# Kernel optimization log

Hardware: AMD Instinct MI355X
Metric: run time of the kernel (lower is better)

The kernel has to match this reference:

```python
import jax, jax.numpy as jnp
import numpy as np

N_NODES = 10000
N_EDGES = 30000
NODE_DIM = 75
BOND_DIM = 16
IN_DIM = 64           # nn_conv_in_dim (also NNConv out channels)
INTERNAL = 128        # nn_conv_internal_dim
FP_DIM = 4096
N_GRAPHS = 16
DEPTH = 3


def _glorot(key, shape):
    fan_in = shape[0]
    return jax.random.normal(key, shape, dtype=jnp.float32) / np.sqrt(fan_in)


def setup_inputs() -> dict:
    key = jax.random.key(0)
    ks = jax.random.split(key, 16)
    x = jax.random.normal(ks[0], (N_NODES, NODE_DIM), dtype=jnp.float32)
    edge_index = jax.random.randint(ks[1], (2, N_EDGES), 0, N_NODES, dtype=jnp.int32)
    edge_attr = jax.random.uniform(ks[2], (N_EDGES, BOND_DIM), dtype=jnp.float32)
    # last column is the bond type flag: 0 = covalent, 1 = spatial
    bond_type = jax.random.randint(ks[3], (N_EDGES,), 0, 2).astype(jnp.float32)
    edge_attr = edge_attr.at[:, -1].set(bond_type)
    batch = jnp.sort(jax.random.randint(ks[4], (N_NODES,), 0, N_GRAPHS, dtype=jnp.int32))
    return {
        "x": x,
        "edge_index": edge_index,
        "edge_attr": edge_attr,
        "batch": batch,
        # atom_expand_nn: Linear(node_dim, nn_conv_in_dim) + ReLU
        "W_ae": _glorot(ks[5], (NODE_DIM, IN_DIM)),
        "b_ae": jnp.zeros((IN_DIM,), jnp.float32),
        # NNConv edge MLP: Linear(bond_dim, internal) -> ReLU -> Linear(internal, in*in)
        "W_e1": _glorot(ks[6], (BOND_DIM, INTERNAL)),
        "b_e1": jnp.zeros((INTERNAL,), jnp.float32),
        "W_e2": _glorot(ks[7], (INTERNAL, IN_DIM * IN_DIM)),
        "b_e2": jnp.zeros((IN_DIM * IN_DIM,), jnp.float32),
        # NNConv root weight + bias
        "W_root": _glorot(ks[8], (IN_DIM, IN_DIM)),
        "b_conv": jnp.zeros((IN_DIM,), jnp.float32),
        # expand_to_fp_nn: Linear(nn_conv_in_dim, fp_dim) + ReLU
        "W_fp": _glorot(ks[9], (IN_DIM, FP_DIM)),
        "b_fp": jnp.zeros((FP_DIM,), jnp.float32),
    }


def reference(x, edge_index, edge_attr, batch,
              W_ae, b_ae, W_e1, b_e1, W_e2, b_e2, W_root, b_conv, W_fp, b_fp):
    src, dst = edge_index[0], edge_index[1]
    cov_mask = (edge_attr[:, -1] == 0.0).astype(x.dtype)   # [E]
    spa_mask = 1.0 - cov_mask

    msg = jax.nn.relu(x @ W_ae + b_ae)                      # [N, IN]
    fingerprint = jnp.zeros((FP_DIM,), x.dtype)

    def masked_mean_aggr(per_edge_msg, mask):
        # NNConv aggregation on the masked edge subset (mean over incoming edges)
        s = jax.ops.segment_sum(per_edge_msg * mask[:, None], dst, num_segments=N_NODES)
        cnt = jax.ops.segment_sum(mask, dst, num_segments=N_NODES)
        return jnp.where(cnt[:, None] > 0, s / jnp.maximum(cnt, 1.0)[:, None], 0.0)

    for _ in range(DEPTH):
        # edge MLP -> per-edge [IN, IN] weight matrix (dropout inactive at eval)
        h = jax.nn.relu(edge_attr @ W_e1 + b_e1)            # [E, INTERNAL]
        w = (h @ W_e2 + b_e2).reshape(N_EDGES, IN_DIM, IN_DIM)
        # gather source features and apply per-edge matrix
        per_edge = jnp.einsum('ei,eio->eo', msg[src], w)    # [E, IN]
        root = msg @ W_root + b_conv                        # [N, IN]
        cov_out = masked_mean_aggr(per_edge, cov_mask) + root
        spa_out = masked_mean_aggr(per_edge, spa_mask) + root
        msg = jax.nn.relu(cov_out + spa_out)
        # expand_to_fp_nn includes ReLU; outer F.relu is idempotent
        expanded = jax.nn.relu(msg @ W_fp + b_fp)           # [N, FP]
        pooled = jax.ops.segment_sum(expanded, batch, num_segments=N_GRAPHS)  # add pool
        # sparsify = identity; skip_connections=True accumulates every depth
        fingerprint = fingerprint + pooled
    return fingerprint                                      # [N_GRAPHS, FP_DIM]
```

## Files before the change

kernel.cpp:

```cpp
#include <hip/hip_runtime.h>
#include <hip/hip_fp16.h>

#define N_NODES 10000
#define N_EDGES 30000
#define NODE_DIM 75
#define BOND_DIM 16
#define IN_DIM 64
#define INTERNAL 128
#define FP_DIM 4096
#define N_GRAPHS 16
#define DEPTH 3

typedef _Float16 half8v __attribute__((ext_vector_type(8)));
typedef float float4v __attribute__((ext_vector_type(4)));

__global__ void k_atom_expand(const float* __restrict__ x, const float* __restrict__ W,
                              const float* __restrict__ b, float* __restrict__ msg,
                              __half* __restrict__ msg16) {
    int n = blockIdx.x;
    int o = threadIdx.x;
    __shared__ float xr[NODE_DIM];
    if (o < NODE_DIM) xr[o] = x[(size_t)n * NODE_DIM + o];
    if (o + 64 < NODE_DIM) xr[o + 64] = x[(size_t)n * NODE_DIM + o + 64];
    __syncthreads();
    float acc = b[o];
    #pragma unroll
    for (int k = 0; k < NODE_DIM; ++k) acc = fmaf(xr[k], W[k * IN_DIM + o], acc);
    float v = fmaxf(acc, 0.f);
    msg[(size_t)n * IN_DIM + o] = v;
    msg16[(size_t)n * IN_DIM + o] = __float2half(v);
}

__global__ void k_edge_h16(const float* __restrict__ ea, const float* __restrict__ W1,
                           const float* __restrict__ b1, __half* __restrict__ h,
                           const int* __restrict__ dst,
                           float* __restrict__ cntC, float* __restrict__ cntS,
                           const int* __restrict__ batch, int* __restrict__ gstart,
                           float* __restrict__ agg0) {
    const int tid = threadIdx.x;
    const int q = tid >> 7;
    const int j = tid & 127;
    const int e = blockIdx.x * 2 + q;
    __shared__ float r[2][BOND_DIM];
    if (j < BOND_DIM) r[q][j] = ea[(size_t)e * BOND_DIM + j];

    if (blockIdx.x < 1250)
        ((float2*)agg0)[(size_t)blockIdx.x * 256 + tid] = (float2){0.f, 0.f};
    if (blockIdx.x == 0 && tid <= N_GRAPHS) {
        int g = tid, lo = 0, hi = N_NODES;
        while (lo < hi) { int mid = (lo + hi) >> 1; if (batch[mid] < g) lo = mid + 1; else hi = mid; }
        gstart[g] = lo;
    }
    __syncthreads();
    if (j == 0) {
        if (r[q][BOND_DIM - 1] == 0.f) atomicAdd(&cntC[dst[e]], 1.f);
        else                           atomicAdd(&cntS[dst[e]], 1.f);
    }
    float acc = b1[j];
    #pragma unroll
    for (int k = 0; k < BOND_DIM; ++k) acc = fmaf(r[q][k], W1[k * INTERNAL + j], acc);
    h[(size_t)e * INTERNAL + j] = __float2half(fmaxf(acc, 0.f));
}

__global__ void k_w2t(const float* __restrict__ W2, __half* __restrict__ W2T) {
    __shared__ _Float16 t[64][136];
    const int tid = threadIdx.x;
    const int n0 = blockIdx.x * 64;
    #pragma unroll
    for (int i = 0; i < 32; ++i) {
        int k = (tid >> 6) + 4 * i;
        int n = tid & 63;
        t[n][k] = (_Float16)W2[(size_t)k * 4096 + n0 + n];
    }
    __syncthreads();
    const int nr = tid >> 2;
    const int kc = (tid & 3) * 32;
    _Float16* dstp = (_Float16*)W2T + (size_t)(n0 + nr) * INTERNAL + kc;
    const _Float16* srcp = &t[nr][kc];
    #pragma unroll
    for (int j = 0; j < 4; ++j)
        *(half8v*)(dstp + 8 * j) = *(const half8v*)(srcp + 8 * j);
}

__global__ void k_wfpt(const float* __restrict__ Wfp, __half* __restrict__ WfpT) {
    __shared__ _Float16 t[64][80];
    const int tid = threadIdx.x;
    const int n0 = blockIdx.x * 64;
    #pragma unroll
    for (int i = 0; i < 16; ++i) {
        int k = (tid >> 6) + 4 * i;
        int n = tid & 63;
        t[n][k] = (_Float16)Wfp[(size_t)k * 4096 + n0 + n];
    }
    __syncthreads();
    const int nr = tid >> 2;
    const int kc = (tid & 3) * 16;
    _Float16* dstp = (_Float16*)WfpT + (size_t)(n0 + nr) * IN_DIM + kc;
    const _Float16* srcp = &t[nr][kc];
    *(half8v*)(dstp)     = *(const half8v*)(srcp);
    *(half8v*)(dstp + 8) = *(const half8v*)(srcp + 8);
}

__global__ __launch_bounds__(512) void k_wgemm(
    const __half* __restrict__ h16, const __half* __restrict__ W2T,
    const float* __restrict__ b2, __half* __restrict__ w)
{
    __shared__ _Float16 B[128][136];
    __shared__ _Float16 st[8][16][136];
    const int tid  = threadIdx.x;
    const int lane = tid & 63;
    const int wv   = tid >> 6;
    const int nbase = blockIdx.x * 128;
    const int ebase = blockIdx.y * 256 + wv * 32;
    const int l15 = lane & 15;
    const int kq  = (lane >> 4) * 8;

    const _Float16* hp = (const _Float16*)h16;
    const _Float16* wp = (const _Float16*)W2T;

    half8v a[2][4];
    #pragma unroll
    for (int mi = 0; mi < 2; ++mi) {
        int e = ebase + mi * 16 + l15;
        if (e >= N_EDGES) e = N_EDGES - 1;
        const _Float16* arow = hp + (size_t)e * INTERNAL;
        #pragma unroll
        for (int kk = 0; kk < 4; ++kk)
            a[mi][kk] = *(const half8v*)(arow + kk * 32 + kq);
    }
    float bias[8];
    #pragma unroll
    for (int ni = 0; ni < 8; ++ni) bias[ni] = b2[nbase + ni * 16 + l15];

    {
        int r  = tid >> 2;
        int c0 = (tid & 3) * 32;
        const _Float16* srcp = wp + (size_t)(nbase + r) * INTERNAL + c0;
        *(half8v*)&B[r][c0]      = *(const half8v*)(srcp);
        *(half8v*)&B[r][c0 + 8]  = *(const half8v*)(srcp + 8);
        *(half8v*)&B[r][c0 + 16] = *(const half8v*)(srcp + 16);
        *(half8v*)&B[r][c0 + 24] = *(const half8v*)(srcp + 24);
    }
    __syncthreads();

    float4v acc[2][8];
    #pragma unroll
    for (int mi = 0; mi < 2; ++mi)
        #pragma unroll
        for (int ni = 0; ni < 8; ++ni)
            acc[mi][ni] = (float4v){0.f, 0.f, 0.f, 0.f};

    #pragma unroll
    for (int kk = 0; kk < 4; ++kk) {
        half8v bw[8];
        #pragma unroll
        for (int ni = 0; ni < 8; ++ni)
            bw[ni] = *(const half8v*)&B[ni * 16 + l15][kk * 32 + kq];
        #pragma unroll
        for (int ni = 0; ni < 8; ++ni) {
            acc[0][ni] = __builtin_amdgcn_mfma_f32_16x16x32_f16(a[0][kk], bw[ni], acc[0][ni], 0, 0, 0);
            acc[1][ni] = __builtin_amdgcn_mfma_f32_16x16x32_f16(a[1][kk], bw[ni], acc[1][ni], 0, 0, 0);
        }
    }

    const int rq = (lane >> 4) * 4;
    #pragma unroll
    for (int mi = 0; mi < 2; ++mi) {
        #pragma unroll
        for (int ni = 0; ni < 8; ++ni)
            #pragma unroll
            for (int r = 0; r < 4; ++r)
                st[wv][rq + r][ni * 16 + l15] = (_Float16)(acc[mi][ni][r] + bias[ni]);
        #pragma unroll
        for (int it = 0; it < 4; ++it) {
            int erow = it * 4 + (lane >> 4);
            half8v v = *(const half8v*)&st[wv][erow][l15 * 8];
            int e = ebase + mi * 16 + erow;
            if (e < N_EDGES)
                *(half8v*)((_Float16*)w + (size_t)e * FP_DIM + nbase + l15 * 8) = v;
        }
    }
}

__global__ __launch_bounds__(256) void k_edge_apply(
    const float* __restrict__ msg, const __half* __restrict__ w,
    const int* __restrict__ src, const int* __restrict__ dst,
    const float* __restrict__ ea,
    const float* __restrict__ cntC, const float* __restrict__ cntS,
    float* __restrict__ agg)
{
    const int lane = threadIdx.x & 63;
    const int ig = lane >> 3;
    const int oc = lane & 7;
    const int nw = (int)gridDim.x * 4;
    int e = (int)blockIdx.x * 4 + ((int)threadIdx.x >> 6);
    if (e >= N_EDGES) return;

    float mv = msg[(size_t)src[e] * IN_DIM + lane];
    half8v w8[8];
    {
        const half8v* wr = (const half8v*)((const _Float16*)w + (size_t)e * FP_DIM);
        #pragma unroll
        for (int t = 0; t < 8; ++t) w8[t] = wr[(ig + 8 * t) * 8 + oc];
    }
    int dv = dst[e];
    float scale = 1.0f / ((ea[(size_t)e * BOND_DIM + (BOND_DIM - 1)] == 0.f)
                          ? cntC[dv] : cntS[dv]);

    while (true) {
        const int en = e + nw;
        const bool has = (en < N_EDGES);
        float nmv = 0.f, nscale = 0.f;
        int ndv = 0;
        half8v n8[8];
        if (has) {
            nmv = msg[(size_t)src[en] * IN_DIM + lane];
            const half8v* wrn = (const half8v*)((const _Float16*)w + (size_t)en * FP_DIM);
            #pragma unroll
            for (int t = 0; t < 8; ++t) n8[t] = wrn[(ig + 8 * t) * 8 + oc];
            ndv = dst[en];
            nscale = 1.0f / ((ea[(size_t)en * BOND_DIM + (BOND_DIM - 1)] == 0.f)
                             ? cntC[ndv] : cntS[ndv]);
        }

        float acc[8] = {0.f, 0.f, 0.f, 0.f, 0.f, 0.f, 0.f, 0.f};
        #pragma unroll
        for (int t = 0; t < 8; ++t) {
            float mi = __shfl(mv, ig + 8 * t);
            #pragma unroll
            for (int j = 0; j < 8; ++j) acc[j] = fmaf(mi, (float)w8[t][j], acc[j]);
        }
        #pragma unroll
        for (int d = 8; d < 64; d <<= 1)
            #pragma unroll
            for (int j = 0; j < 8; ++j) acc[j] += __shfl_xor(acc[j], d);

        float v = (ig == 0) ? acc[0] : (ig == 1) ? acc[1] : (ig == 2) ? acc[2] :
                  (ig == 3) ? acc[3] : (ig == 4) ? acc[4] : (ig == 5) ? acc[5] :
                  (ig == 6) ? acc[6] : acc[7];
        atomicAdd(&agg[(size_t)dv * IN_DIM + oc * 8 + ig], v * scale);

        if (!has) break;
        e = en; mv = nmv; dv = ndv; scale = nscale;
        #pragma unroll
        for (int t = 0; t < 8; ++t) w8[t] = n8[t];
    }
}

__global__ void k_combine(const float* __restrict__ msg_old, const float* __restrict__ Wr,
                          const float* __restrict__ bc,
                          float* __restrict__ agg,
                          float* __restrict__ msg_new, __half* __restrict__ msg16) {
    int tid = threadIdx.x;
    int n = blockIdx.x * 4 + (tid >> 6);
    int o = tid & 63;
    int q = tid >> 6;
    __shared__ float r[4][IN_DIM];
    r[q][o] = msg_old[(size_t)n * IN_DIM + o];
    __syncthreads();
    float root = bc[o];
    #pragma unroll
    for (int k = 0; k < IN_DIM; ++k) root = fmaf(r[q][k], Wr[k * IN_DIM + o], root);
    size_t idx = (size_t)n * IN_DIM + o;
    float a = agg[idx];
    agg[idx] = 0.f;
    float v = fmaxf(a + 2.f * root, 0.f);
    msg_new[idx] = v;
    msg16[idx] = __float2half(v);
}

__global__ __launch_bounds__(256) void k_fp_pool_mfma(
    const __half* __restrict__ msg16, const __half* __restrict__ WfpT,
    const float* __restrict__ bfp, const int* __restrict__ gstart,
    float* __restrict__ out)
{
    const int tid = threadIdx.x, lane = tid & 63, wid = tid >> 6;
    const int g = blockIdx.y;
    const int cbase = blockIdx.x * 256 + wid * 64;
    const int l15 = lane & 15;
    const int kq = (lane >> 4) * 8;
    const int rq = (lane >> 4) * 4;

    const _Float16* wt = (const _Float16*)WfpT;
    const _Float16* mp = (const _Float16*)msg16;

    half8v bf[4][2];
    float bias[4];
    #pragma unroll
    for (int nf = 0; nf < 4; ++nf) {
        int n = cbase + nf * 16 + l15;
        #pragma unroll
        for (int kk = 0; kk < 2; ++kk)
            bf[nf][kk] = *(const half8v*)(wt + (size_t)n * IN_DIM + kk * 32 + kq);
        bias[nf] = bfp[n];
    }

    int n0g = gstart[g], n1g = gstart[g + 1];
    int len = n1g - n0g;
    int chunk = (len + (int)gridDim.z - 1) / (int)gridDim.z;
    int rs = n0g + (int)blockIdx.z * chunk;
    int re = min(rs + chunk, n1g);
    if (rs >= re) return;

    float pool[4] = {0.f, 0.f, 0.f, 0.f};
    int node0 = rs + l15; if (node0 >= n1g) node0 = n1g - 1;
    half8v af0 = *(const half8v*)(mp + (size_t)node0 * IN_DIM + kq);
    half8v af1 = *(const half8v*)(mp + (size_t)node0 * IN_DIM + 32 + kq);
    for (int r = rs; r < re; r += 16) {
        half8v nf0 = af0, nf1 = af1;
        if (r + 16 < re) {
            int node = r + 16 + l15; if (node >= n1g) node = n1g - 1;
            nf0 = *(const half8v*)(mp + (size_t)node * IN_DIM + kq);
            nf1 = *(const half8v*)(mp + (size_t)node * IN_DIM + 32 + kq);
        }
        #pragma unroll
        for (int nf = 0; nf < 4; ++nf) {
            float4v d = (float4v){0.f, 0.f, 0.f, 0.f};
            d = __builtin_amdgcn_mfma_f32_16x16x32_f16(af0, bf[nf][0], d, 0, 0, 0);
            d = __builtin_amdgcn_mfma_f32_16x16x32_f16(af1, bf[nf][1], d, 0, 0, 0);
            #pragma unroll
            for (int reg = 0; reg < 4; ++reg) {
                int rr = r + rq + reg;
                if (rr < re) pool[nf] += fmaxf(d[reg] + bias[nf], 0.f);
            }
        }
        af0 = nf0; af1 = nf1;
    }
    #pragma unroll
    for (int nf = 0; nf < 4; ++nf) {
        pool[nf] += __shfl_xor(pool[nf], 16);
        pool[nf] += __shfl_xor(pool[nf], 32);
    }
    if (lane < 16) {
        #pragma unroll
        for (int nf = 0; nf < 4; ++nf)
            atomicAdd(&out[(size_t)g * FP_DIM + cbase + nf * 16 + lane], pool[nf]);
    }
}

extern "C" void kernel_launch(void* const* d_in, const int* in_sizes, int n_in,
                              void* d_out, int out_size, void* d_ws, size_t ws_size,
                              hipStream_t stream) {
    const float* x        = (const float*)d_in[0];
    const int*   eidx     = (const int*)d_in[1];
    const float* ea       = (const float*)d_in[2];
    const int*   batch    = (const int*)d_in[3];
    const float* W_ae     = (const float*)d_in[4];
    const float* b_ae     = (const float*)d_in[5];
    const float* W_e1     = (const float*)d_in[6];
    const float* b_e1     = (const float*)d_in[7];
    const float* W_e2     = (const float*)d_in[8];
    const float* b_e2     = (const float*)d_in[9];
    const float* W_root   = (const float*)d_in[10];
    const float* b_conv   = (const float*)d_in[11];
    const float* W_fp     = (const float*)d_in[12];
    const float* b_fp     = (const float*)d_in[13];
    const int* src = eidx;
    const int* dst = eidx + N_EDGES;
    float* out = (float*)d_out;

    hipMemsetAsync(out, 0, (size_t)out_size * sizeof(float), stream);

    float* ws   = (float*)d_ws;
    float* msgA = ws;
    float* msgB = msgA + 640000;
    float* aggC = msgB + 640000;
    float* aggS = aggC + 640000;
    float* cntC = aggS + 640000;
    float* cntS = cntC + 10000;
    int*   gst  = (int*)(cntS + 10000);

    __half* h16   = (__half*)(gst + 32);
    __half* W2T   = h16 + (size_t)N_EDGES * INTERNAL;
    __half* wbig  = W2T + (size_t)FP_DIM * INTERNAL;
    __half* msg16 = wbig + (size_t)N_EDGES * FP_DIM;
    __half* WfpT  = msg16 + (size_t)N_NODES * IN_DIM;

    size_t need = (4ull * 640000 + 2 * 10000 + 32) * 4
                + ((size_t)N_EDGES * INTERNAL + (size_t)FP_DIM * INTERNAL
                   + (size_t)N_EDGES * FP_DIM + (size_t)N_NODES * IN_DIM
                   + (size_t)FP_DIM * IN_DIM) * 2;
    if (ws_size < need) return;

    hipMemsetAsync(cntC, 0, 2 * (size_t)N_NODES * sizeof(float), stream);
    k_atom_expand<<<N_NODES, 64, 0, stream>>>(x, W_ae, b_ae, msgA, msg16);
    k_edge_h16<<<N_EDGES / 2, 256, 0, stream>>>(ea, W_e1, b_e1, h16,
                                                dst, cntC, cntS, batch, gst, aggC);
    k_w2t<<<64, 256, 0, stream>>>(W_e2, W2T);
    k_wfpt<<<64, 256, 0, stream>>>(W_fp, WfpT);
    k_wgemm<<<dim3(FP_DIM / 128, (N_EDGES + 255) / 256), 512, 0, stream>>>(
        h16, W2T, b_e2, wbig);

    float* cur = msgA;
    float* nxt = msgB;
    for (int d = 0; d < DEPTH; ++d) {
        k_edge_apply<<<1024, 256, 0, stream>>>(
            cur, wbig, src, dst, ea, cntC, cntS, aggC);
        k_combine<<<N_NODES / 4, 256, 0, stream>>>(cur, W_root, b_conv, aggC,
                                                   nxt, msg16);
        k_fp_pool_mfma<<<dim3(FP_DIM / 256, N_GRAPHS, 8), 256, 0, stream>>>(
            msg16, WfpT, b_fp, gst, out);
        float* t = cur; cur = nxt; nxt = t;
    }
}
```

Baseline: 309.9 us.

## Batch node expand blocks, merge transposes, shrink staging, double-buffer edge apply

The atom-expand kernel now handles four nodes per 256-thread block instead of one node per 64-thread block. The two weight-transpose kernels are merged into one launch. The wgemm epilogue stages the output through a half-size shared buffer in four passes, which lowers LDS use and may allow more resident blocks. The edge-apply loop becomes a two-deep software pipeline with A/B register sets, and the fp-pool grid z dimension drops from 8 to 4. Together these aim to cut launch overhead, improve occupancy and hide load latency, at the cost of more registers in edge_apply.

```diff
diff --git a/kernel.cpp b/kernel.cpp
--- a/kernel.cpp
+++ b/kernel.cpp
@@ -17,15 +17,17 @@
 __global__ void k_atom_expand(const float* __restrict__ x, const float* __restrict__ W,
                               const float* __restrict__ b, float* __restrict__ msg,
                               __half* __restrict__ msg16) {
-    int n = blockIdx.x;
-    int o = threadIdx.x;
-    __shared__ float xr[NODE_DIM];
-    if (o < NODE_DIM) xr[o] = x[(size_t)n * NODE_DIM + o];
-    if (o + 64 < NODE_DIM) xr[o + 64] = x[(size_t)n * NODE_DIM + o + 64];
+    int tid = threadIdx.x;
+    int q = tid >> 6;
+    int o = tid & 63;
+    int n = blockIdx.x * 4 + q;
+    __shared__ float xr[4][NODE_DIM];
+    if (o < NODE_DIM) xr[q][o] = x[(size_t)n * NODE_DIM + o];
+    if (o + 64 < NODE_DIM) xr[q][o + 64] = x[(size_t)n * NODE_DIM + o + 64];
     __syncthreads();
     float acc = b[o];
     #pragma unroll
-    for (int k = 0; k < NODE_DIM; ++k) acc = fmaf(xr[k], W[k * IN_DIM + o], acc);
+    for (int k = 0; k < NODE_DIM; ++k) acc = fmaf(xr[q][k], W[k * IN_DIM + o], acc);
     float v = fmaxf(acc, 0.f);
     msg[(size_t)n * IN_DIM + o] = v;
     msg16[(size_t)n * IN_DIM + o] = __float2half(v);
@@ -62,43 +64,42 @@
     h[(size_t)e * INTERNAL + j] = __float2half(fmaxf(acc, 0.f));
 }
 
-__global__ void k_w2t(const float* __restrict__ W2, __half* __restrict__ W2T) {
+__global__ void k_wt(const float* __restrict__ W2, const float* __restrict__ Wfp,
+                     __half* __restrict__ W2T, __half* __restrict__ WfpT) {
     __shared__ _Float16 t[64][136];
     const int tid = threadIdx.x;
-    const int n0 = blockIdx.x * 64;
-    #pragma unroll
-    for (int i = 0; i < 32; ++i) {
-        int k = (tid >> 6) + 4 * i;
-        int n = tid & 63;
-        t[n][k] = (_Float16)W2[(size_t)k * 4096 + n0 + n];
-    }
-    __syncthreads();
-    const int nr = tid >> 2;
-    const int kc = (tid & 3) * 32;
-    _Float16* dstp = (_Float16*)W2T + (size_t)(n0 + nr) * INTERNAL + kc;
-    const _Float16* srcp = &t[nr][kc];
-    #pragma unroll
-    for (int j = 0; j < 4; ++j)
-        *(half8v*)(dstp + 8 * j) = *(const half8v*)(srcp + 8 * j);
-}
-
-__global__ void k_wfpt(const float* __restrict__ Wfp, __half* __restrict__ WfpT) {
-    __shared__ _Float16 t[64][80];
-    const int tid = threadIdx.x;
-    const int n0 = blockIdx.x * 64;
-    #pragma unroll
-    for (int i = 0; i < 16; ++i) {
-        int k = (tid >> 6) + 4 * i;
-        int n = tid & 63;
-        t[n][k] = (_Float16)Wfp[(size_t)k * 4096 + n0 + n];
-    }
-    __syncthreads();
-    const int nr = tid >> 2;
-    const int kc = (tid & 3) * 16;
-    _Float16* dstp = (_Float16*)WfpT + (size_t)(n0 + nr) * IN_DIM + kc;
-    const _Float16* srcp = &t[nr][kc];
-    *(half8v*)(dstp)     = *(const half8v*)(srcp);
-    *(half8v*)(dstp + 8) = *(const half8v*)(srcp + 8);
+    if (blockIdx.x < 64) {
+        const int n0 = blockIdx.x * 64;
+        #pragma unroll
+        for (int i = 0; i < 32; ++i) {
+            int k = (tid >> 6) + 4 * i;
+            int n = tid & 63;
+            t[n][k] = (_Float16)W2[(size_t)k * 4096 + n0 + n];
+        }
+        __syncthreads();
+        const int nr = tid >> 2;
+        const int kc = (tid & 3) * 32;
+        _Float16* dstp = (_Float16*)W2T + (size_t)(n0 + nr) * INTERNAL + kc;
+        const _Float16* srcp = &t[nr][kc];
+        #pragma unroll
+        for (int j = 0; j < 4; ++j)
+            *(half8v*)(dstp + 8 * j) = *(const half8v*)(srcp + 8 * j);
+    } else {
+        const int n0 = (blockIdx.x - 64) * 64;
+        #pragma unroll
+        for (int i = 0; i < 16; ++i) {
+            int k = (tid >> 6) + 4 * i;
+            int n = tid & 63;
+            t[n][k] = (_Float16)Wfp[(size_t)k * 4096 + n0 + n];
+        }
+        __syncthreads();
+        const int nr = tid >> 2;
+        const int kc = (tid & 3) * 16;
+        _Float16* dstp = (_Float16*)WfpT + (size_t)(n0 + nr) * IN_DIM + kc;
+        const _Float16* srcp = &t[nr][kc];
+        *(half8v*)(dstp)     = *(const half8v*)(srcp);
+        *(half8v*)(dstp + 8) = *(const half8v*)(srcp + 8);
+    }
 }
 
 __global__ __launch_bounds__(512) void k_wgemm(
@@ -106,7 +107,7 @@
     const float* __restrict__ b2, __half* __restrict__ w)
 {
     __shared__ _Float16 B[128][136];
-    __shared__ _Float16 st[8][16][136];
+    __shared__ _Float16 st[8][8][136];
     const int tid  = threadIdx.x;
     const int lane = tid & 63;
     const int wv   = tid >> 6;
@@ -114,6 +115,7 @@
     const int ebase = blockIdx.y * 256 + wv * 32;
     const int l15 = lane & 15;
     const int kq  = (lane >> 4) * 8;
+    const int g   = lane >> 4;
 
     const _Float16* hp = (const _Float16*)h16;
     const _Float16* wp = (const _Float16*)W2T;
@@ -163,19 +165,23 @@
         }
     }
 
-    const int rq = (lane >> 4) * 4;
-    #pragma unroll
-    for (int mi = 0; mi < 2; ++mi) {
-        #pragma unroll
-        for (int ni = 0; ni < 8; ++ni)
+    #pragma unroll
+    for (int pass = 0; pass < 4; ++pass) {
+        const int mi = pass >> 1;
+        const int half = (pass & 1) * 8;
+        if ((g >> 1) == (pass & 1)) {
+            int rowInPass = g * 4 - half;
             #pragma unroll
-            for (int r = 0; r < 4; ++r)
-                st[wv][rq + r][ni * 16 + l15] = (_Float16)(acc[mi][ni][r] + bias[ni]);
-        #pragma unroll
-        for (int it = 0; it < 4; ++it) {
-            int erow = it * 4 + (lane >> 4);
+            for (int ni = 0; ni < 8; ++ni)
+                #pragma unroll
+                for (int r = 0; r < 4; ++r)
+                    st[wv][rowInPass + r][ni * 16 + l15] = (_Float16)(acc[mi][ni][r] + bias[ni]);
+        }
+        #pragma unroll
+        for (int it = 0; it < 2; ++it) {
+            int erow = it * 4 + g;
             half8v v = *(const half8v*)&st[wv][erow][l15 * 8];
-            int e = ebase + mi * 16 + erow;
+            int e = ebase + mi * 16 + half + erow;
             if (e < N_EDGES)
                 *(half8v*)((_Float16*)w + (size_t)e * FP_DIM + nbase + l15 * 8) = v;
         }
@@ -196,33 +202,16 @@
     int e = (int)blockIdx.x * 4 + ((int)threadIdx.x >> 6);
     if (e >= N_EDGES) return;
 
-    float mv = msg[(size_t)src[e] * IN_DIM + lane];
-    half8v w8[8];
-    {
-        const half8v* wr = (const half8v*)((const _Float16*)w + (size_t)e * FP_DIM);
+    auto LOAD = [&](int ee, float& mv, half8v* w8, int& dv, float& sc) {
+        mv = msg[(size_t)src[ee] * IN_DIM + lane];
+        const half8v* wr = (const half8v*)((const _Float16*)w + (size_t)ee * FP_DIM);
         #pragma unroll
         for (int t = 0; t < 8; ++t) w8[t] = wr[(ig + 8 * t) * 8 + oc];
-    }
-    int dv = dst[e];
-    float scale = 1.0f / ((ea[(size_t)e * BOND_DIM + (BOND_DIM - 1)] == 0.f)
-                          ? cntC[dv] : cntS[dv]);
-
-    while (true) {
-        const int en = e + nw;
-        const bool has = (en < N_EDGES);
-        float nmv = 0.f, nscale = 0.f;
-        int ndv = 0;
-        half8v n8[8];
-        if (has) {
-            nmv = msg[(size_t)src[en] * IN_DIM + lane];
-            const half8v* wrn = (const half8v*)((const _Float16*)w + (size_t)en * FP_DIM);
-            #pragma unroll
-            for (int t = 0; t < 8; ++t) n8[t] = wrn[(ig + 8 * t) * 8 + oc];
-            ndv = dst[en];
-            nscale = 1.0f / ((ea[(size_t)en * BOND_DIM + (BOND_DIM - 1)] == 0.f)
-                             ? cntC[ndv] : cntS[ndv]);
-        }
-
+        dv = dst[ee];
+        sc = 1.0f / ((ea[(size_t)ee * BOND_DIM + (BOND_DIM - 1)] == 0.f)
+                     ? cntC[dv] : cntS[dv]);
+    };
+    auto PROC = [&](float mv, const half8v* w8, int dv, float sc) {
         float acc[8] = {0.f, 0.f, 0.f, 0.f, 0.f, 0.f, 0.f, 0.f};
         #pragma unroll
         for (int t = 0; t < 8; ++t) {
@@ -234,16 +223,29 @@
         for (int d = 8; d < 64; d <<= 1)
             #pragma unroll
             for (int j = 0; j < 8; ++j) acc[j] += __shfl_xor(acc[j], d);
-
         float v = (ig == 0) ? acc[0] : (ig == 1) ? acc[1] : (ig == 2) ? acc[2] :
                   (ig == 3) ? acc[3] : (ig == 4) ? acc[4] : (ig == 5) ? acc[5] :
                   (ig == 6) ? acc[6] : acc[7];
-        atomicAdd(&agg[(size_t)dv * IN_DIM + oc * 8 + ig], v * scale);
-
-        if (!has) break;
-        e = en; mv = nmv; dv = ndv; scale = nscale;
-        #pragma unroll
-        for (int t = 0; t < 8; ++t) w8[t] = n8[t];
+        atomicAdd(&agg[(size_t)dv * IN_DIM + oc * 8 + ig], v * sc);
+    };
+
+    float mvA, scA; int dvA; half8v wA[8];
+    float mvB, scB; int dvB; half8v wB[8];
+    LOAD(e, mvA, wA, dvA, scA);
+    bool hasB = (e + nw < N_EDGES);
+    if (hasB) LOAD(e + nw, mvB, wB, dvB, scB);
+
+    while (true) {
+        bool hasC = (e + 2 * nw < N_EDGES);
+        PROC(mvA, wA, dvA, scA);
+        if (hasC) LOAD(e + 2 * nw, mvA, wA, dvA, scA);
+        if (!hasB) break;
+        bool hasD = (e + 3 * nw < N_EDGES);
+        PROC(mvB, wB, dvB, scB);
+        if (hasD) LOAD(e + 3 * nw, mvB, wB, dvB, scB);
+        if (!hasC) break;
+        e += 2 * nw;
+        hasB = hasD;
     }
 }
 
@@ -383,11 +385,10 @@
     if (ws_size < need) return;
 
     hipMemsetAsync(cntC, 0, 2 * (size_t)N_NODES * sizeof(float), stream);
-    k_atom_expand<<<N_NODES, 64, 0, stream>>>(x, W_ae, b_ae, msgA, msg16);
+    k_atom_expand<<<N_NODES / 4, 256, 0, stream>>>(x, W_ae, b_ae, msgA, msg16);
     k_edge_h16<<<N_EDGES / 2, 256, 0, stream>>>(ea, W_e1, b_e1, h16,
                                                 dst, cntC, cntS, batch, gst, aggC);
-    k_w2t<<<64, 256, 0, stream>>>(W_e2, W2T);
-    k_wfpt<<<64, 256, 0, stream>>>(W_fp, WfpT);
+    k_wt<<<128, 256, 0, stream>>>(W_e2, W_fp, W2T, WfpT);
     k_wgemm<<<dim3(FP_DIM / 128, (N_EDGES + 255) / 256), 512, 0, stream>>>(
         h16, W2T, b_e2, wbig);
 
@@ -398,7 +399,7 @@
             cur, wbig, src, dst, ea, cntC, cntS, aggC);
         k_combine<<<N_NODES / 4, 256, 0, stream>>>(cur, W_root, b_conv, aggC,
                                                    nxt, msg16);
-        k_fp_pool_mfma<<<dim3(FP_DIM / 256, N_GRAPHS, 8), 256, 0, stream>>>(
+        k_fp_pool_mfma<<<dim3(FP_DIM / 256, N_GRAPHS, 4), 256, 0, stream>>>(
             msg16, WfpT, b_fp, gst, out);
         float* t = cur; cur = nxt; nxt = t;
     }
```

Measured after the change: 314.2 us. No clear change (+1.4%).
